# Optimization experiments

Hardware: AMD Instinct MI355X
Metric: run time of the kernel (lower is better)

The kernel has to match this reference:

```python
import jax, jax.numpy as jnp
import numpy as np

TAU = 2.0  # gumbel-softmax temperature (hard=False)


def setup_inputs() -> dict:
    key = jax.random.key(0)
    k = jax.random.split(key, 6)
    b = 128
    names = jax.random.normal(k[0], (b, 256, 30, 32), jnp.float32)
    patterns = jax.random.normal(k[1], (b, 4, 128, 128), jnp.float32)
    attributes = jax.random.normal(k[2], (b, 8, 15, 16), jnp.float32)
    palettes = jax.random.normal(k[3], (b, 8, 12), jnp.float32)
    u1 = jax.random.uniform(k[4], (b, 960, 256), jnp.float32, 1e-6, 1.0 - 1e-6)
    u2 = jax.random.uniform(k[5], (b, 240, 8), jnp.float32, 1e-6, 1.0 - 1e-6)
    gumbel_names = -jnp.log(-jnp.log(u1))
    gumbel_attrs = -jnp.log(-jnp.log(u2))
    return {"names": names, "patterns": patterns, "attributes": attributes,
            "palettes": palettes, "gumbel_names": gumbel_names, "gumbel_attrs": gumbel_attrs}


def reference(names, patterns, attributes, palettes, gumbel_names, gumbel_attrs):
    b = names.shape[0]
    # tile-name logits: (b,256,30,32) -> (b, 960 tiles, 256 names)
    n = names.reshape(b, 256, 30 * 32).transpose(0, 2, 1)
    names_idxs = jax.nn.softmax((n + gumbel_names) / TAU, axis=-1)
    # pattern table: (b,4,128,128) -> 256 tiles of 8x8 pixels x 4 gray levels
    p = patterns.reshape(b, 4, 16, 8, 16, 8).transpose(0, 2, 4, 3, 5, 1)
    p = jax.nn.softmax(p, axis=-1).reshape(b, 256, 8 * 8 * 4)
    # attribute logits: (b,8,15,16) -> (b, 240 blocks, 8 palettes)
    a = attributes.reshape(b, 8, 15 * 16).transpose(0, 2, 1)
    attributes_idxs = jax.nn.softmax((a + gumbel_attrs) / TAU, axis=-1)
    pal = palettes.reshape(b, 8, 4 * 3)
    # soft tile lookup: (b,960,256) @ (b,256,256) -> (b,960,256)
    monochrome = jnp.einsum('btn,bnp->btp', names_idxs, p)
    monochrome = monochrome.reshape(b, 30 * 32, 8 * 8, 4, 1)
    # soft palette lookup: (b,240,8) @ (b,8,12) -> (b,240,12)
    colorization = jnp.einsum('bte,bec->btc', attributes_idxs, pal)
    colorization = colorization.reshape(b, 15, 16, 4, 3)
    # 2x2 attribute-block broadcast to the 30x32 nametable
    colorization = jnp.repeat(jnp.repeat(colorization, 2, axis=1), 2, axis=2)
    colorization = colorization.reshape(b, 30 * 32, 1, 4, 3)
    colorized = (monochrome * colorization).sum(axis=3)  # (b,960,64,3)
    image = colorized.reshape(b, 30, 32, 8, 8, 3).transpose(0, 5, 1, 3, 2, 4)
    image = image.reshape(b, 3, 30 * 8, 32 * 8)
    image = jax.nn.sigmoid(image)
    return image, names_idxs, p, attributes_idxs, pal
```

## Files before the change

### kernel.cpp

```cpp
#include <hip/hip_runtime.h>
#include <hip/hip_bf16.h>
#include <math.h>

#define O_IMG   0
#define O_NAMES 23592960ULL
#define O_P     55050240ULL
#define O_ATTR  63438848ULL
#define O_PAL   63684608ULL

typedef __attribute__((ext_vector_type(8))) short short8v;
typedef __attribute__((ext_vector_type(4))) float f32x4;

static __device__ inline unsigned short f2bf(float x) {
    __hip_bfloat16 h = __float2bfloat16(x);
    return *reinterpret_cast<unsigned short*>(&h);
}

template<bool WRITE_PT>
__global__ __launch_bounds__(256) void k_pattern_t(const float* __restrict__ patterns,
                                                   float* __restrict__ out_p,
                                                   unsigned short* __restrict__ Pt) {
    int idx = blockIdx.x * 256 + threadIdx.x;
    int col = idx & 127;
    int row = (idx >> 7) & 127;
    int b   = idx >> 14;
    const float* base = patterns + (size_t)b * 65536 + row * 128 + col;
    float v0 = base[0];
    float v1 = base[16384];
    float v2 = base[2 * 16384];
    float v3 = base[3 * 16384];
    float m = fmaxf(fmaxf(v0, v1), fmaxf(v2, v3));
    float e0 = expf(v0 - m), e1 = expf(v1 - m), e2 = expf(v2 - m), e3 = expf(v3 - m);
    float inv = 1.0f / (e0 + e1 + e2 + e3);
    float p0 = e0 * inv, p1 = e1 * inv, p2 = e2 * inv, p3 = e3 * inv;
    int ti = row >> 3, pi = row & 7, tj = col >> 3, pj = col & 7;
    int n  = ti * 16 + tj;
    int px = pi * 8 + pj;
    size_t o = ((size_t)(b * 256 + n) * 64 + px) * 4;
    float4 r; r.x = p0; r.y = p1; r.z = p2; r.w = p3;
    *(float4*)(out_p + o) = r;
    if (WRITE_PT) {
        unsigned short* pt = Pt + (size_t)b * 65536 + (size_t)(px * 4) * 256 + n;
        pt[0]   = f2bf(p0);
        pt[256] = f2bf(p1);
        pt[512] = f2bf(p2);
        pt[768] = f2bf(p3);
    }
}

__global__ __launch_bounds__(256) void k_names(const float* __restrict__ names,
                                               const float* __restrict__ gumbel,
                                               float* __restrict__ out) {
    int chunk = blockIdx.x % 60;
    int b     = blockIdx.x / 60;
    int t0 = chunk * 16;
    __shared__ float sN[256 * 17];

    int q = threadIdx.x;
    const float* nb = names + (size_t)b * 245760 + t0;
    {
        int j  = q & 3;
        int n0 = q >> 2;
        #pragma unroll
        for (int pass = 0; pass < 4; pass++) {
            int n = n0 + 64 * pass;
            float4 v = *(const float4*)(nb + (size_t)n * 960 + 4 * j);
            float* dst = sN + n * 17 + 4 * j;
            dst[0] = v.x; dst[1] = v.y; dst[2] = v.z; dst[3] = v.w;
        }
    }
    __syncthreads();

    int lane = q & 63;
    int w    = q >> 6;
    const float* gb = gumbel + ((size_t)b * 960 + t0) * 256;
    float*       ob = out    + ((size_t)b * 960 + t0) * 256;

    #pragma unroll
    for (int tt = 0; tt < 4; tt++) {
        int t = w * 4 + tt;
        float v[4];
        #pragma unroll
        for (int k = 0; k < 4; k++) {
            int n = lane + 64 * k;
            v[k] = (sN[n * 17 + t] + gb[(size_t)t * 256 + n]) * 0.5f;
        }
        float m = fmaxf(fmaxf(v[0], v[1]), fmaxf(v[2], v[3]));
        #pragma unroll
        for (int off = 1; off < 64; off <<= 1) m = fmaxf(m, __shfl_xor(m, off));
        float s = 0.f;
        #pragma unroll
        for (int k = 0; k < 4; k++) { v[k] = expf(v[k] - m); s += v[k]; }
        #pragma unroll
        for (int off = 1; off < 64; off <<= 1) s += __shfl_xor(s, off);
        float inv = 1.0f / s;
        #pragma unroll
        for (int k = 0; k < 4; k++) ob[(size_t)t * 256 + lane + 64 * k] = v[k] * inv;
    }
}

__global__ __launch_bounds__(256) void k_attr(const float* __restrict__ attributes,
                                              const float* __restrict__ gumbel,
                                              const float* __restrict__ palettes,
                                              float* __restrict__ out_attr,
                                              float* __restrict__ out_pal) {
    int idx = blockIdx.x * 256 + threadIdx.x;
    if (idx < 12288) out_pal[idx] = palettes[idx];
    if (idx >= 128 * 240) return;
    int tb = idx % 240;
    int b  = idx / 240;
    float v[8];
    float m = -1e30f;
    #pragma unroll
    for (int e = 0; e < 8; e++) {
        v[e] = (attributes[((size_t)b * 8 + e) * 240 + tb] +
                gumbel[((size_t)b * 240 + tb) * 8 + e]) * 0.5f;
        m = fmaxf(m, v[e]);
    }
    float s = 0.f;
    #pragma unroll
    for (int e = 0; e < 8; e++) { v[e] = expf(v[e] - m); s += v[e]; }
    float inv = 1.0f / s;
    float* o = out_attr + (size_t)idx * 8;
    #pragma unroll
    for (int e = 0; e < 8; e++) o[e] = v[e] * inv;
}

__global__ __launch_bounds__(256) void k_image_mfma(const float* __restrict__ A,
                                                    const unsigned short* __restrict__ Pt,
                                                    const float* __restrict__ attr,
                                                    const float* __restrict__ pal,
                                                    float* __restrict__ img) {
    int j  = blockIdx.x;
    int x  = j & 7;
    int s  = j >> 3;
    int q  = s / 15;
    int rr = s % 15;
    int b  = x + 8 * q;
    int t0 = rr * 64;

    __shared__ __align__(16) char smem[32768];
    __shared__ float sCol[192];

    int tid = threadIdx.x;

    if (tid < 192) {
        int tbl = tid / 12;
        int gc  = tid % 12;
        int tb  = rr * 16 + tbl;
        const float* at = attr + ((size_t)b * 240 + tb) * 8;
        const float* pl = pal + (size_t)b * 96 + gc;
        float sum = 0.f;
        #pragma unroll
        for (int e = 0; e < 8; e++) sum += at[e] * pl[e * 12];
        sCol[tbl * 12 + gc] = sum;
    }

    {
        const float* Ab = A + ((size_t)b * 960 + t0) * 256;
        int t  = tid >> 2;
        int kb = (tid & 3) * 64;
        #pragma unroll
        for (int jj = 0; jj < 8; jj++) {
            int k = kb + jj * 8;
            float4 u0 = *(const float4*)(Ab + (size_t)t * 256 + k);
            float4 u1 = *(const float4*)(Ab + (size_t)t * 256 + k + 4);
            short8v h;
            h[0] = f2bf(u0.x); h[1] = f2bf(u0.y); h[2] = f2bf(u0.z); h[3] = f2bf(u0.w);
            h[4] = f2bf(u1.x); h[5] = f2bf(u1.y); h[6] = f2bf(u1.z); h[7] = f2bf(u1.w);
            int off = (t * 512 + k * 2) ^ ((t & 7) << 4);
            *(short8v*)(smem + off) = h;
        }
    }
    __syncthreads();

    f32x4 acc[4][4];
    #pragma unroll
    for (int mi = 0; mi < 4; mi++)
        #pragma unroll
        for (int ni = 0; ni < 4; ni++) acc[mi][ni] = (f32x4){0.f, 0.f, 0.f, 0.f};

    int lane = tid & 63;
    int w    = tid >> 6;
    int lo   = lane & 15;
    int hi   = lane >> 4;

    const unsigned short* Ptb = Pt + (size_t)b * 65536 + hi * 8;

    short8v bcur[4], bnxt[4];
    #pragma unroll
    for (int ni = 0; ni < 4; ni++) {
        int f = w * 64 + ni * 16 + lo;
        bcur[ni] = *(const short8v*)(Ptb + (size_t)f * 256);
    }

    #pragma unroll
    for (int k0 = 0; k0 < 256; k0 += 32) {
        if (k0 < 224) {
            #pragma unroll
            for (int ni = 0; ni < 4; ni++) {
                int f = w * 64 + ni * 16 + lo;
                bnxt[ni] = *(const short8v*)(Ptb + (size_t)f * 256 + k0 + 32);
            }
        }
        int ka = (k0 + hi * 8) * 2;
        short8v a0 = *(short8v*)(smem + (((lo      ) * 512 + ka) ^ ((lo & 7) << 4)));
        short8v a1 = *(short8v*)(smem + (((lo + 16) * 512 + ka) ^ ((lo & 7) << 4)));
        short8v a2 = *(short8v*)(smem + (((lo + 32) * 512 + ka) ^ ((lo & 7) << 4)));
        short8v a3 = *(short8v*)(smem + (((lo + 48) * 512 + ka) ^ ((lo & 7) << 4)));
        #pragma unroll
        for (int ni = 0; ni < 4; ni++) {
            acc[0][ni] = __builtin_amdgcn_mfma_f32_16x16x32_bf16(a0, bcur[ni], acc[0][ni], 0, 0, 0);
            acc[1][ni] = __builtin_amdgcn_mfma_f32_16x16x32_bf16(a1, bcur[ni], acc[1][ni], 0, 0, 0);
            acc[2][ni] = __builtin_amdgcn_mfma_f32_16x16x32_bf16(a2, bcur[ni], acc[2][ni], 0, 0, 0);
            acc[3][ni] = __builtin_amdgcn_mfma_f32_16x16x32_bf16(a3, bcur[ni], acc[3][ni], 0, 0, 0);
        }
        if (k0 < 224) {
            #pragma unroll
            for (int ni = 0; ni < 4; ni++) bcur[ni] = bnxt[ni];
        }
    }

    float* sMono = (float*)smem;
    int tf = tid & 63;
    int tm = tid >> 6;
    int pi = tf >> 3, pj = tf & 7;

    #pragma unroll
    for (int mi = 0; mi < 4; mi++) {
        __syncthreads();
        #pragma unroll
        for (int ni = 0; ni < 4; ni++) {
            int colf = w * 64 + ni * 16 + lo;
            #pragma unroll
            for (int rg = 0; rg < 4; rg++)
                sMono[(hi * 4 + rg) * 260 + colf] = acc[mi][ni][rg];
        }
        __syncthreads();
        int r    = rr * 2 + (mi >> 1);
        int cbase = (mi & 1) * 16;
        #pragma unroll
        for (int i = 0; i < 4; i++) {
            int ccl  = tm * 4 + i;
            int ccol = cbase + ccl;
            int tbl  = ccol >> 1;
            float4 mv = *(float4*)&sMono[ccl * 260 + tf * 4];
            #pragma unroll
            for (int c = 0; c < 3; c++) {
                float sv = mv.x * sCol[tbl * 12 + c]
                         + mv.y * sCol[tbl * 12 + 3 + c]
                         + mv.z * sCol[tbl * 12 + 6 + c]
                         + mv.w * sCol[tbl * 12 + 9 + c];
                float y = 1.0f / (1.0f + expf(-sv));
                img[(((size_t)b * 3 + c) * 240 + r * 8 + pi) * 256 + ccol * 8 + pj] = y;
            }
        }
    }
}

__global__ __launch_bounds__(256) void k_image_fp32(const float* __restrict__ A,
                                                    const float* __restrict__ P,
                                                    const float* __restrict__ attr,
                                                    const float* __restrict__ pal,
                                                    float* __restrict__ img) {
    int blk = blockIdx.x;
    int r = blk % 30;
    int b = blk / 30;
    int t0 = r * 32;

    __shared__ float sA[32][33];
    __shared__ float sB[32][256];
    __shared__ float sColF[16][12];

    int tid = threadIdx.x;
    if (tid < 192) {
        int tbl = tid / 12;
        int gc  = tid % 12;
        int tb  = (r >> 1) * 16 + tbl;
        const float* at = attr + ((size_t)b * 240 + tb) * 8;
        const float* pl = pal + (size_t)b * 96 + gc;
        float s = 0.f;
        #pragma unroll
        for (int e = 0; e < 8; e++) s += at[e] * pl[e * 12];
        sColF[tbl][gc] = s;
    }

    float acc[8][4];
    #pragma unroll
    for (int i = 0; i < 8; i++)
        #pragma unroll
        for (int j = 0; j < 4; j++) acc[i][j] = 0.f;

    int tf = tid & 63;
    int tm = tid >> 6;

    const float* Ab = A + ((size_t)b * 960 + t0) * 256;
    const float* Pb = P + (size_t)b * 65536;

    for (int k0 = 0; k0 < 256; k0 += 32) {
        __syncthreads();
        #pragma unroll
        for (int i = 0; i < 4; i++) {
            int li = tid + i * 256;
            int tl = li >> 5, kk = li & 31;
            sA[tl][kk] = Ab[(size_t)tl * 256 + k0 + kk];
        }
        #pragma unroll
        for (int i = 0; i < 8; i++) {
            int li = tid + i * 256;
            int kk = li >> 6, ff = (li & 63) * 4;
            *(float4*)&sB[kk][ff] = *(const float4*)&Pb[(size_t)(k0 + kk) * 256 + ff];
        }
        __syncthreads();
        #pragma unroll
        for (int kk = 0; kk < 32; kk++) {
            float4 bv = *(float4*)&sB[kk][tf * 4];
            #pragma unroll
            for (int i = 0; i < 8; i++) {
                float av = sA[tm * 8 + i][kk];
                acc[i][0] += av * bv.x;
                acc[i][1] += av * bv.y;
                acc[i][2] += av * bv.z;
                acc[i][3] += av * bv.w;
            }
        }
    }

    int pi = tf >> 3, pj = tf & 7;
    #pragma unroll
    for (int i = 0; i < 8; i++) {
        int cc  = tm * 8 + i;
        int tbl = cc >> 1;
        #pragma unroll
        for (int c = 0; c < 3; c++) {
            float s = acc[i][0] * sColF[tbl][c]
                    + acc[i][1] * sColF[tbl][3 + c]
                    + acc[i][2] * sColF[tbl][6 + c]
                    + acc[i][3] * sColF[tbl][9 + c];
            float y = 1.0f / (1.0f + expf(-s));
            img[(((size_t)b * 3 + c) * 240 + r * 8 + pi) * 256 + cc * 8 + pj] = y;
        }
    }
}

extern "C" void kernel_launch(void* const* d_in, const int* in_sizes, int n_in,
                              void* d_out, int out_size, void* d_ws, size_t ws_size,
                              hipStream_t stream) {
    const float* names       = (const float*)d_in[0];
    const float* patterns    = (const float*)d_in[1];
    const float* attributes  = (const float*)d_in[2];
    const float* palettes    = (const float*)d_in[3];
    const float* gumbel_n    = (const float*)d_in[4];
    const float* gumbel_a    = (const float*)d_in[5];
    float* out = (float*)d_out;

    float* out_img   = out + O_IMG;
    float* out_names = out + O_NAMES;
    float* out_p     = out + O_P;
    float* out_attr  = out + O_ATTR;
    float* out_pal   = out + O_PAL;

    const size_t PT_BYTES = 128ULL * 256 * 256 * 2;
    bool use_mfma = (ws_size >= PT_BYTES) && (d_ws != nullptr);

    if (use_mfma) {
        unsigned short* Pt = (unsigned short*)d_ws;
        k_pattern_t<true><<<8192, 256, 0, stream>>>(patterns, out_p, Pt);
        k_names<<<128 * 60, 256, 0, stream>>>(names, gumbel_n, out_names);
        k_attr<<<120, 256, 0, stream>>>(attributes, gumbel_a, palettes, out_attr, out_pal);
        k_image_mfma<<<1920, 256, 0, stream>>>(out_names, Pt, out_attr, palettes, out_img);
    } else {
        k_pattern_t<false><<<8192, 256, 0, stream>>>(patterns, out_p, nullptr);
        k_names<<<128 * 60, 256, 0, stream>>>(names, gumbel_n, out_names);
        k_attr<<<120, 256, 0, stream>>>(attributes, gumbel_a, palettes, out_attr, out_pal);
        k_image_fp32<<<128 * 30, 256, 0, stream>>>(out_names, out_p, out_attr, palettes, out_img);
    }
}
```

Before: 185.8 us.

## Swap MFMA operand order to apply colorization directly from accumulator registers

Swaps the MFMA A/B operands so each lane's accumulator holds the four gray-level channels of one pixel for one tile. The epilogue can then apply the palette mix and sigmoid straight from registers, which removes the shared-memory staging of the monochrome result and its per-mi __syncthreads barriers. The palette table is padded to a 16-float stride so each lane reads it with float4 loads. In exchange the image stores become scattered per-lane scalar writes, which may coalesce worse than before.

```diff
diff --git a/kernel.cpp b/kernel.cpp
--- a/kernel.cpp
+++ b/kernel.cpp
@@ -140,7 +140,7 @@
     int t0 = rr * 64;
 
     __shared__ __align__(16) char smem[32768];
-    __shared__ float sCol[192];
+    __shared__ float sColP[16 * 16];
 
     int tid = threadIdx.x;
 
@@ -153,7 +153,7 @@
         float sum = 0.f;
         #pragma unroll
         for (int e = 0; e < 8; e++) sum += at[e] * pl[e * 12];
-        sCol[tbl * 12 + gc] = sum;
+        sColP[tbl * 16 + gc] = sum;
     }
 
     {
@@ -176,9 +176,9 @@
 
     f32x4 acc[4][4];
     #pragma unroll
-    for (int mi = 0; mi < 4; mi++)
-        #pragma unroll
-        for (int ni = 0; ni < 4; ni++) acc[mi][ni] = (f32x4){0.f, 0.f, 0.f, 0.f};
+    for (int fi = 0; fi < 4; fi++)
+        #pragma unroll
+        for (int ti = 0; ti < 4; ti++) acc[fi][ti] = (f32x4){0.f, 0.f, 0.f, 0.f};
 
     int lane = tid & 63;
     int w    = tid >> 6;
@@ -189,18 +189,18 @@
 
     short8v bcur[4], bnxt[4];
     #pragma unroll
-    for (int ni = 0; ni < 4; ni++) {
-        int f = w * 64 + ni * 16 + lo;
-        bcur[ni] = *(const short8v*)(Ptb + (size_t)f * 256);
+    for (int fi = 0; fi < 4; fi++) {
+        int f = w * 64 + fi * 16 + lo;
+        bcur[fi] = *(const short8v*)(Ptb + (size_t)f * 256);
     }
 
     #pragma unroll
     for (int k0 = 0; k0 < 256; k0 += 32) {
         if (k0 < 224) {
             #pragma unroll
-            for (int ni = 0; ni < 4; ni++) {
-                int f = w * 64 + ni * 16 + lo;
-                bnxt[ni] = *(const short8v*)(Ptb + (size_t)f * 256 + k0 + 32);
+            for (int fi = 0; fi < 4; fi++) {
+                int f = w * 64 + fi * 16 + lo;
+                bnxt[fi] = *(const short8v*)(Ptb + (size_t)f * 256 + k0 + 32);
             }
         }
         int ka = (k0 + hi * 8) * 2;
@@ -209,51 +209,44 @@
         short8v a2 = *(short8v*)(smem + (((lo + 32) * 512 + ka) ^ ((lo & 7) << 4)));
         short8v a3 = *(short8v*)(smem + (((lo + 48) * 512 + ka) ^ ((lo & 7) << 4)));
         #pragma unroll
-        for (int ni = 0; ni < 4; ni++) {
-            acc[0][ni] = __builtin_amdgcn_mfma_f32_16x16x32_bf16(a0, bcur[ni], acc[0][ni], 0, 0, 0);
-            acc[1][ni] = __builtin_amdgcn_mfma_f32_16x16x32_bf16(a1, bcur[ni], acc[1][ni], 0, 0, 0);
-            acc[2][ni] = __builtin_amdgcn_mfma_f32_16x16x32_bf16(a2, bcur[ni], acc[2][ni], 0, 0, 0);
-            acc[3][ni] = __builtin_amdgcn_mfma_f32_16x16x32_bf16(a3, bcur[ni], acc[3][ni], 0, 0, 0);
+        for (int fi = 0; fi < 4; fi++) {
+            acc[fi][0] = __builtin_amdgcn_mfma_f32_16x16x32_bf16(bcur[fi], a0, acc[fi][0], 0, 0, 0);
+            acc[fi][1] = __builtin_amdgcn_mfma_f32_16x16x32_bf16(bcur[fi], a1, acc[fi][1], 0, 0, 0);
+            acc[fi][2] = __builtin_amdgcn_mfma_f32_16x16x32_bf16(bcur[fi], a2, acc[fi][2], 0, 0, 0);
+            acc[fi][3] = __builtin_amdgcn_mfma_f32_16x16x32_bf16(bcur[fi], a3, acc[fi][3], 0, 0, 0);
         }
         if (k0 < 224) {
             #pragma unroll
-            for (int ni = 0; ni < 4; ni++) bcur[ni] = bnxt[ni];
-        }
-    }
-
-    float* sMono = (float*)smem;
-    int tf = tid & 63;
-    int tm = tid >> 6;
-    int pi = tf >> 3, pj = tf & 7;
-
-    #pragma unroll
-    for (int mi = 0; mi < 4; mi++) {
-        __syncthreads();
-        #pragma unroll
-        for (int ni = 0; ni < 4; ni++) {
-            int colf = w * 64 + ni * 16 + lo;
-            #pragma unroll
-            for (int rg = 0; rg < 4; rg++)
-                sMono[(hi * 4 + rg) * 260 + colf] = acc[mi][ni][rg];
-        }
-        __syncthreads();
-        int r    = rr * 2 + (mi >> 1);
-        int cbase = (mi & 1) * 16;
-        #pragma unroll
-        for (int i = 0; i < 4; i++) {
-            int ccl  = tm * 4 + i;
-            int ccol = cbase + ccl;
-            int tbl  = ccol >> 1;
-            float4 mv = *(float4*)&sMono[ccl * 260 + tf * 4];
-            #pragma unroll
-            for (int c = 0; c < 3; c++) {
-                float sv = mv.x * sCol[tbl * 12 + c]
-                         + mv.y * sCol[tbl * 12 + 3 + c]
-                         + mv.z * sCol[tbl * 12 + 6 + c]
-                         + mv.w * sCol[tbl * 12 + 9 + c];
-                float y = 1.0f / (1.0f + expf(-sv));
-                img[(((size_t)b * 3 + c) * 240 + r * 8 + pi) * 256 + ccol * 8 + pj] = y;
-            }
+            for (int fi = 0; fi < 4; fi++) bcur[fi] = bnxt[fi];
+        }
+    }
+
+    float* ib = img + (size_t)b * 184320;
+    #pragma unroll
+    for (int ti = 0; ti < 4; ti++) {
+        int tl   = ti * 16 + lo;
+        int tbl  = (tl & 31) >> 1;
+        float4 c0 = *(float4*)&sColP[tbl * 16 + 0];
+        float4 c1 = *(float4*)&sColP[tbl * 16 + 4];
+        float4 c2 = *(float4*)&sColP[tbl * 16 + 8];
+        int r    = rr * 2 + (tl >> 5);
+        int ccol = tl & 31;
+        float* tb_ = ib + (size_t)(r * 8) * 256 + ccol * 8;
+        #pragma unroll
+        for (int fi = 0; fi < 4; fi++) {
+            int px = w * 16 + fi * 4 + hi;
+            int pi = px >> 3, pj = px & 7;
+            f32x4 a4 = acc[fi][ti];
+            float s0 = a4[0] * c0.x + a4[1] * c0.w + a4[2] * c1.z + a4[3] * c2.y;
+            float s1 = a4[0] * c0.y + a4[1] * c1.x + a4[2] * c1.w + a4[3] * c2.z;
+            float s2 = a4[0] * c0.z + a4[1] * c1.y + a4[2] * c2.x + a4[3] * c2.w;
+            float y0 = 1.0f / (1.0f + expf(-s0));
+            float y1 = 1.0f / (1.0f + expf(-s1));
+            float y2 = 1.0f / (1.0f + expf(-s2));
+            size_t poff = (size_t)(pi * 256 + pj);
+            tb_[poff]              = y0;
+            tb_[61440 + poff]      = y1;
+            tb_[2 * 61440 + poff]  = y2;
         }
     }
 }
```

Result: slower. 204.1 us (+9.8%).

## Fuse names gumbel-softmax into the MFMA image kernel

Applied to the files above, without the earlier changes.

Removes the separate k_names launch and computes the names softmax inside the image kernel. Each block transposes its 64-tile slice of names through padded shared memory, adds gumbel noise, does a wave-wide shuffle softmax, writes the fp32 result to the output and stores the bf16 copy straight into the swizzled A tile. This avoids writing names_idxs and then reading it back from global memory, and drops one launch. In exchange it adds about 17KB of shared memory per block, a launch_bounds occupancy hint, and strided 960-element loads from names inside the GEMM kernel.

```diff
diff --git a/kernel.cpp b/kernel.cpp
--- a/kernel.cpp
+++ b/kernel.cpp
@@ -126,11 +126,13 @@
     for (int e = 0; e < 8; e++) o[e] = v[e] * inv;
 }
 
-__global__ __launch_bounds__(256) void k_image_mfma(const float* __restrict__ A,
-                                                    const unsigned short* __restrict__ Pt,
-                                                    const float* __restrict__ attr,
-                                                    const float* __restrict__ pal,
-                                                    float* __restrict__ img) {
+__global__ __launch_bounds__(256, 3) void k_fused(const float* __restrict__ names,
+                                                  const float* __restrict__ gumbel,
+                                                  const unsigned short* __restrict__ Pt,
+                                                  const float* __restrict__ attr,
+                                                  const float* __restrict__ pal,
+                                                  float* __restrict__ out_names,
+                                                  float* __restrict__ img) {
     int j  = blockIdx.x;
     int x  = j & 7;
     int s  = j >> 3;
@@ -140,9 +142,14 @@
     int t0 = rr * 64;
 
     __shared__ __align__(16) char smem[32768];
+    __shared__ float sN[256 * 17];
     __shared__ float sCol[192];
 
-    int tid = threadIdx.x;
+    int tid  = threadIdx.x;
+    int lane = tid & 63;
+    int w    = tid >> 6;
+    int lo   = lane & 15;
+    int hi   = lane >> 4;
 
     if (tid < 192) {
         int tbl = tid / 12;
@@ -156,20 +163,50 @@
         sCol[tbl * 12 + gc] = sum;
     }
 
-    {
-        const float* Ab = A + ((size_t)b * 960 + t0) * 256;
-        int t  = tid >> 2;
-        int kb = (tid & 3) * 64;
-        #pragma unroll
-        for (int jj = 0; jj < 8; jj++) {
-            int k = kb + jj * 8;
-            float4 u0 = *(const float4*)(Ab + (size_t)t * 256 + k);
-            float4 u1 = *(const float4*)(Ab + (size_t)t * 256 + k + 4);
-            short8v h;
-            h[0] = f2bf(u0.x); h[1] = f2bf(u0.y); h[2] = f2bf(u0.z); h[3] = f2bf(u0.w);
-            h[4] = f2bf(u1.x); h[5] = f2bf(u1.y); h[6] = f2bf(u1.z); h[7] = f2bf(u1.w);
-            int off = (t * 512 + k * 2) ^ ((t & 7) << 4);
-            *(short8v*)(smem + off) = h;
+    const float* nb  = names + (size_t)b * 245760 + t0;
+    const float* gb  = gumbel + ((size_t)b * 960 + t0) * 256;
+    float*       onb = out_names + ((size_t)b * 960 + t0) * 256;
+
+    for (int c = 0; c < 4; c++) {
+        if (c) __syncthreads();
+        {
+            int jj = tid & 3;
+            int n0 = tid >> 2;
+            #pragma unroll
+            for (int p = 0; p < 4; p++) {
+                int n = n0 + 64 * p;
+                float4 v = *(const float4*)(nb + (size_t)n * 960 + c * 16 + 4 * jj);
+                float* dst = sN + n * 17 + 4 * jj;
+                dst[0] = v.x; dst[1] = v.y; dst[2] = v.z; dst[3] = v.w;
+            }
+        }
+        __syncthreads();
+        #pragma unroll
+        for (int tt = 0; tt < 4; tt++) {
+            int trow = w * 4 + tt;
+            int tl   = c * 16 + trow;
+            float v[4];
+            #pragma unroll
+            for (int k = 0; k < 4; k++) {
+                int n = lane + 64 * k;
+                v[k] = (sN[n * 17 + trow] + gb[(size_t)tl * 256 + n]) * 0.5f;
+            }
+            float m = fmaxf(fmaxf(v[0], v[1]), fmaxf(v[2], v[3]));
+            #pragma unroll
+            for (int off = 1; off < 64; off <<= 1) m = fmaxf(m, __shfl_xor(m, off));
+            float sm = 0.f;
+            #pragma unroll
+            for (int k = 0; k < 4; k++) { v[k] = expf(v[k] - m); sm += v[k]; }
+            #pragma unroll
+            for (int off = 1; off < 64; off <<= 1) sm += __shfl_xor(sm, off);
+            float inv = 1.0f / sm;
+            #pragma unroll
+            for (int k = 0; k < 4; k++) {
+                int n = lane + 64 * k;
+                float p = v[k] * inv;
+                onb[(size_t)tl * 256 + n] = p;
+                *(unsigned short*)(smem + ((tl * 512 + n * 2) ^ ((tl & 7) << 4))) = f2bf(p);
+            }
         }
     }
     __syncthreads();
@@ -179,11 +216,6 @@
     for (int mi = 0; mi < 4; mi++)
         #pragma unroll
         for (int ni = 0; ni < 4; ni++) acc[mi][ni] = (f32x4){0.f, 0.f, 0.f, 0.f};
-
-    int lane = tid & 63;
-    int w    = tid >> 6;
-    int lo   = lane & 15;
-    int hi   = lane >> 4;
 
     const unsigned short* Ptb = Pt + (size_t)b * 65536 + hi * 8;
 
@@ -237,7 +269,7 @@
                 sMono[(hi * 4 + rg) * 260 + colf] = acc[mi][ni][rg];
         }
         __syncthreads();
-        int r    = rr * 2 + (mi >> 1);
+        int r     = rr * 2 + (mi >> 1);
         int cbase = (mi & 1) * 16;
         #pragma unroll
         for (int i = 0; i < 4; i++) {
@@ -366,9 +398,9 @@
     if (use_mfma) {
         unsigned short* Pt = (unsigned short*)d_ws;
         k_pattern_t<true><<<8192, 256, 0, stream>>>(patterns, out_p, Pt);
-        k_names<<<128 * 60, 256, 0, stream>>>(names, gumbel_n, out_names);
         k_attr<<<120, 256, 0, stream>>>(attributes, gumbel_a, palettes, out_attr, out_pal);
-        k_image_mfma<<<1920, 256, 0, stream>>>(out_names, Pt, out_attr, palettes, out_img);
+        k_fused<<<1920, 256, 0, stream>>>(names, gumbel_n, Pt, out_attr, palettes,
+                                          out_names, out_img);
     } else {
         k_pattern_t<false><<<8192, 256, 0, stream>>>(patterns, out_p, nullptr);
         k_names<<<128 * 60, 256, 0, stream>>>(names, gumbel_n, out_names);
```

Measured after the change: 168.8 us. 9.1% less time.
